# Kernel optimization log

Hardware: AMD Instinct MI355X
Metric: run time of the kernel (lower is better)

## Reference

```python
import jax, jax.numpy as jnp
import numpy as np

N = 100000  # nodes
E = 1600000  # edges
D_IN, D_HID, D_OUT = 128, 128, 64
NEG_SLOPE = 0.2


def gat_conv(x, src, dst, W_src, W_dst, att_src, att_dst, bias, num_nodes):
    # PyG GATConv, heads=1, add_self_loops=False.
    h_src = x @ W_src          # [N, C]
    h_dst = x @ W_dst          # [N, C]
    a_src = (h_src * att_src).sum(-1)   # [N]
    a_dst = (h_dst * att_dst).sum(-1)   # [N]
    logits = jax.nn.leaky_relu(a_src[src] + a_dst[dst], NEG_SLOPE)  # [E]
    # segment softmax over destination neighborhoods
    seg_max = jax.ops.segment_max(logits, dst, num_segments=num_nodes)  # [N]
    e = jnp.exp(logits - seg_max[dst])
    denom = jax.ops.segment_sum(e, dst, num_segments=num_nodes)         # [N]
    alpha = e / (denom[dst] + 1e-16)                                    # [E]
    out = jax.ops.segment_sum(alpha[:, None] * h_src[src], dst, num_segments=num_nodes)  # [N, C]
    return out + bias


def setup_inputs() -> dict:
    key = jax.random.key(0)
    ks = jax.random.split(key, 12)
    x = jax.random.normal(ks[0], (N, D_IN), dtype=jnp.float32)
    edge_index = jax.random.randint(ks[1], (2, E), 0, N, dtype=jnp.int64)
    s1 = 1.0 / np.sqrt(D_IN)
    s2 = 1.0 / np.sqrt(D_HID)
    return {
        "x": x,
        "edge_index": edge_index,
        "W1_src": jax.random.uniform(ks[2], (D_IN, D_HID), jnp.float32, -s1, s1),
        "W1_dst": jax.random.uniform(ks[3], (D_IN, D_HID), jnp.float32, -s1, s1),
        "att1_src": jax.random.uniform(ks[4], (D_HID,), jnp.float32, -s2, s2),
        "att1_dst": jax.random.uniform(ks[5], (D_HID,), jnp.float32, -s2, s2),
        "b1": jnp.zeros((D_HID,), jnp.float32),
        "W2_src": jax.random.uniform(ks[6], (D_HID, D_OUT), jnp.float32, -s2, s2),
        "W2_dst": jax.random.uniform(ks[7], (D_HID, D_OUT), jnp.float32, -s2, s2),
        "att2_src": jax.random.uniform(ks[8], (D_OUT,), jnp.float32, -1.0 / np.sqrt(D_OUT), 1.0 / np.sqrt(D_OUT)),
        "att2_dst": jax.random.uniform(ks[9], (D_OUT,), jnp.float32, -1.0 / np.sqrt(D_OUT), 1.0 / np.sqrt(D_OUT)),
        "b2": jnp.zeros((D_OUT,), jnp.float32),
    }


def reference(x, edge_index, W1_src, W1_dst, att1_src, att1_dst, b1,
              W2_src, W2_dst, att2_src, att2_dst, b2):
    src, dst = edge_index[0], edge_index[1]
    h = gat_conv(x, src, dst, W1_src, W1_dst, att1_src, att1_dst, b1, N)
    h = jax.nn.relu(h)
    out = gat_conv(h, src, dst, W2_src, W2_dst, att2_src, att2_dst, b2, N)
    return out
```

## Files before the change

kernel.cpp:

```cpp
#include <hip/hip_runtime.h>


typedef unsigned long long u64;
typedef float v4f __attribute__((ext_vector_type(4)));
typedef _Float16 v2h __attribute__((ext_vector_type(2)));
typedef __fp16 h8 __attribute__((ext_vector_type(8)));

#define SEL_LO 0x01000504u
#define SEL_HI 0x03020706u

__device__ __forceinline__ void ntstore4(float* p, v4f v) {
    __builtin_nontemporal_store(v, (v4f*)p);
}
__device__ __forceinline__ unsigned h2pack(float a, float b) {
    v2h h;
    h.x = (_Float16)a;
    h.y = (_Float16)b;
    return __builtin_bit_cast(unsigned, h);
}
__device__ __forceinline__ float fdot2u(unsigned u, v2h w, float acc) {
    return __builtin_amdgcn_fdot2(__builtin_bit_cast(v2h, u), w, acc, false);
}
__device__ __forceinline__ v2h pkrtz(float a, float b) {
    return __builtin_bit_cast(v2h, __builtin_amdgcn_cvt_pkrtz(a, b));
}

__global__ __launch_bounds__(64) void matvec_kernel(const float* __restrict__ W,
                                                    const float* __restrict__ a,
                                                    float* __restrict__ out, int cols) {
    int row = blockIdx.x;
    int lane = threadIdx.x;
    float s = 0.f;
    for (int j = lane; j < cols; j += 64) s += W[row * cols + j] * a[j];
#pragma unroll
    for (int o = 32; o; o >>= 1) s += __shfl_xor(s, o, 64);
    if (lane == 0) out[row] = s;
}

template <int C>
__global__ __launch_bounds__(256) void packw_kernel(const float* __restrict__ W,
                                                    uint4* __restrict__ Wp) {
    constexpr int NT = C / 16;
    const int total = 4 * NT * 64;
    for (int e = threadIdx.x; e < total; e += 256) {
        int lane = e & 63;
        int ti = (e >> 6) % NT;
        int t = (e >> 6) / NT;
        int k0 = 32 * t + (lane >> 4) * 8;
        int n = ti * 16 + (lane & 15);
        unsigned u[4];
#pragma unroll
        for (int p = 0; p < 4; ++p)
            u[p] = h2pack(W[(size_t)(k0 + 2 * p) * C + n], W[(size_t)(k0 + 2 * p + 1) * C + n]);
        Wp[e] = make_uint4(u[0], u[1], u[2], u[3]);
    }
}

__global__ __launch_bounds__(256) void bhist_kernel(const int* __restrict__ dst,
                                                    int* __restrict__ gh, int E) {
    __shared__ int h[256];
    h[threadIdx.x] = 0;
    __syncthreads();
    int base = blockIdx.x * 4096;
    int lim = min(base + 4096, E);
    for (int i = base + threadIdx.x; i < lim; i += 256)
        atomicAdd(&h[__builtin_nontemporal_load(dst + i) >> 9], 1);
    __syncthreads();
    int v = h[threadIdx.x];
    if (v) atomicAdd(&gh[threadIdx.x], v);
}

__global__ __launch_bounds__(256) void bscan_kernel(const int* __restrict__ gh,
                                                    int* __restrict__ bbase,
                                                    int* __restrict__ gcur,
                                                    int* __restrict__ offs, int N, int E) {
    __shared__ int s[256];
    int t = threadIdx.x;
    int v = gh[t];
    s[t] = v;
    __syncthreads();
    for (int o = 1; o < 256; o <<= 1) {
        int u = (t >= o) ? s[t - o] : 0;
        __syncthreads();
        s[t] += u;
        __syncthreads();
    }
    int excl = s[t] - v;
    bbase[t] = excl;
    gcur[t] = excl;
    if (t == 255) { bbase[256] = E; offs[N] = E; }
}

__global__ __launch_bounds__(256) void bscatter_kernel(const int* __restrict__ src,
                                                       const int* __restrict__ dst,
                                                       int* __restrict__ gcur,
                                                       u64* __restrict__ pairs, int E) {
    __shared__ int h[256];
    __shared__ int sbase[256];
    __shared__ int rbase[256];
    __shared__ u64 buf[4096];
    const int tid = threadIdx.x;
    h[tid] = 0;
    __syncthreads();
    const int base = blockIdx.x * 4096;
    const int lim = min(4096, E - base);
    u64 pv[16];
    int rk[16];
    int bk[16];
#pragma unroll 16
    for (int k = 0; k < 16; ++k) {
        int i = base + k * 256 + tid;
        if (i < E) {
            int d = __builtin_nontemporal_load(dst + i);
            int b = d >> 9;
            bk[k] = b;
            pv[k] = ((u64)(unsigned)d << 32) | (unsigned)__builtin_nontemporal_load(src + i);
            rk[k] = atomicAdd(&h[b], 1);
        } else {
            bk[k] = -1;
        }
    }
    __syncthreads();
    const int v = h[tid];
    sbase[tid] = v;
    __syncthreads();
    for (int o = 1; o < 256; o <<= 1) {
        int uu = (tid >= o) ? sbase[tid - o] : 0;
        __syncthreads();
        sbase[tid] += uu;
        __syncthreads();
    }
    const int excl = sbase[tid] - v;
    rbase[tid] = v ? atomicAdd(&gcur[tid], v) : 0;
    __syncthreads();
    sbase[tid] = excl;
    __syncthreads();
#pragma unroll 16
    for (int k = 0; k < 16; ++k)
        if (bk[k] >= 0) buf[sbase[bk[k]] + rk[k]] = pv[k];
    __syncthreads();
    for (int i = tid; i < lim; i += 256) {
        u64 p = buf[i];
        int b = (int)(p >> 41);
        __builtin_nontemporal_store(p, pairs + (size_t)rbase[b] + (i - sbase[b]));
    }
}

__global__ __launch_bounds__(512) void bsort_kernel(const u64* __restrict__ pairs,
                                                    const int* __restrict__ bbase,
                                                    int* __restrict__ offs,
                                                    int* __restrict__ srcs, int N) {
    __shared__ int h[512];
    __shared__ int cur[512];
    const int t = threadIdx.x;
    const int b = blockIdx.x;
    const int beg = bbase[b], end = bbase[b + 1];
    h[t] = 0;
    __syncthreads();
    for (int i = beg + t; i < end; i += 512)
        atomicAdd(&h[(int)(__builtin_nontemporal_load(pairs + i) >> 32) & 511], 1);
    __syncthreads();
    int v = h[t];
    cur[t] = v;
    __syncthreads();
    for (int o = 1; o < 512; o <<= 1) {
        int u = (t >= o) ? cur[t - o] : 0;
        __syncthreads();
        cur[t] += u;
        __syncthreads();
    }
    int pos0 = beg + cur[t] - v;
    __syncthreads();
    cur[t] = pos0;
    int g = (b << 9) + t;
    if (g < N) offs[g] = pos0;
    __syncthreads();
    for (int i = beg + t; i < end; i += 512) {
        u64 p = __builtin_nontemporal_load(pairs + i);
        int local = (int)(p >> 32) & 511;
        int pp = atomicAdd(&cur[local], 1);
        srcs[pp] = (int)(p & 0xffffffffu);
    }
}

template <int C, bool XF16>
__global__ __launch_bounds__(256) void gemm_att_kernel(
    const void* __restrict__ Xv, const uint4* __restrict__ Wp,
    const float* __restrict__ attS, const float* __restrict__ wda,
    unsigned* __restrict__ H, float* __restrict__ aS, float* __restrict__ aD, int M) {
    constexpr int NT = C / 16;
    __shared__ _Float16 hs[4][16 * 136];

    const int tid = threadIdx.x;
    const int w = tid >> 6;
    const int lane = tid & 63;
    const int l15 = lane & 15;
    const int q = lane >> 4;
    const int mb = blockIdx.x * 64 + w * 16;
    const int m = mb + l15;
    const bool mv = m < M;

    v4f acc[NT];
#pragma unroll
    for (int n = 0; n < NT; ++n) acc[n] = (v4f)(0.f);
    float pd = 0.f;
    uint4 afu[4];

    if constexpr (XF16) {
        const uint4* Xp = (const uint4*)Xv + (size_t)m * 16;
#pragma unroll
        for (int t = 0; t < 4; ++t) {
            uint4 u = make_uint4(0u, 0u, 0u, 0u);
            if (mv) u = Xp[4 * t + q];
            afu[t] = u;
            const float* wdp = wda + 32 * t + 8 * q;
            pd = fdot2u(u.x, pkrtz(wdp[0], wdp[1]), pd);
            pd = fdot2u(u.y, pkrtz(wdp[2], wdp[3]), pd);
            pd = fdot2u(u.z, pkrtz(wdp[4], wdp[5]), pd);
            pd = fdot2u(u.w, pkrtz(wdp[6], wdp[7]), pd);
        }
    } else {
        const float* Xp = (const float*)Xv + (size_t)m * 128;
#pragma unroll
        for (int t = 0; t < 4; ++t) {
            float4 x0 = make_float4(0.f, 0.f, 0.f, 0.f);
            float4 x1 = x0;
            if (mv) {
                x0 = *(const float4*)(Xp + 32 * t + 8 * q);
                x1 = *(const float4*)(Xp + 32 * t + 8 * q + 4);
            }
            const float* wdp = wda + 32 * t + 8 * q;
            pd += x0.x * wdp[0] + x0.y * wdp[1] + x0.z * wdp[2] + x0.w * wdp[3] +
                  x1.x * wdp[4] + x1.y * wdp[5] + x1.z * wdp[6] + x1.w * wdp[7];
            afu[t] = make_uint4(h2pack(x0.x, x0.y), h2pack(x0.z, x0.w),
                                h2pack(x1.x, x1.y), h2pack(x1.z, x1.w));
        }
    }

#pragma unroll
    for (int t = 0; t < 4; ++t) {
        h8 a = __builtin_bit_cast(h8, afu[t]);
        const uint4* wp = Wp + (size_t)t * NT * 64 + lane;
#pragma unroll
        for (int n = 0; n < NT; ++n) {
            h8 b = __builtin_bit_cast(h8, wp[n * 64]);
            acc[n] = __builtin_amdgcn_mfma_f32_16x16x32_f16(a, b, acc[n], 0, 0, 0);
        }
    }

    pd += __shfl_xor(pd, 16, 64);
    pd += __shfl_xor(pd, 32, 64);
    if (q == 0 && mv) aD[m] = pd;

    float as4[4] = {0.f, 0.f, 0.f, 0.f};
#pragma unroll
    for (int n = 0; n < NT; ++n) {
        float av = attS[n * 16 + l15];
#pragma unroll
        for (int r = 0; r < 4; ++r) as4[r] += acc[n][r] * av;
    }
#pragma unroll
    for (int r = 0; r < 4; ++r) {
#pragma unroll
        for (int o = 1; o < 16; o <<= 1) as4[r] += __shfl_xor(as4[r], o, 64);
    }
    if (l15 == 0) {
#pragma unroll
        for (int r = 0; r < 4; ++r) {
            int row = mb + q * 4 + r;
            if (row < M) aS[row] = as4[r];
        }
    }

    _Float16* hp = hs[w];
#pragma unroll
    for (int n = 0; n < NT; ++n)
#pragma unroll
        for (int r = 0; r < 4; ++r)
            hp[(q * 4 + r) * 136 + n * 16 + l15] = (_Float16)acc[n][r];

    constexpr int CH = C / 32;
    if (lane < 16 * CH) {
        int row = lane / CH;
        int ch = lane % CH;
        const uint4* rp = (const uint4*)(hp + row * 136 + ch * 32);
        uint4 v0 = rp[0], v1 = rp[1], v2 = rp[2], v3 = rp[3];
        int gr = mb + row;
        if (gr < M) {
            uint4* op = (uint4*)(H + (size_t)gr * (C / 2)) + ch * 4;
            op[0] = v0; op[1] = v1; op[2] = v2; op[3] = v3;
        }
    }
}

template <int C, bool RELU, bool F16OUT, bool NTOUT>
__global__ __launch_bounds__(256) void aggregate_kernel(
    const int* __restrict__ offs, const int* __restrict__ srcs,
    const unsigned* __restrict__ hsrc, const float* __restrict__ aS,
    const float* __restrict__ aD, const float* __restrict__ bias,
    void* __restrict__ outv, int n) {
    const int lane = threadIdx.x & 63;
    const int sl = lane & 31;
    const int hb = lane & 32;
    const int g = (lane >> 4) & 1;
    const int l = lane & 15;
    int node = (int)((blockIdx.x * blockDim.x + threadIdx.x) >> 5);
    if (node >= n) return;

    const int beg = offs[node], end = offs[node + 1];
    const int deg = end - beg;
    const float ad = aD[node];

    constexpr int LW = C / 32;
    constexpr int NA = C / 16;
    float acc[NA];
#pragma unroll
    for (int i = 0; i < NA; ++i) acc[i] = 0.f;

    int sj = 0;
    float u = 0.f;

    auto ldrow = [&](int s, unsigned* r) {
        if constexpr (C == 128) {
            uint4 v = ((const uint4*)(hsrc + ((size_t)s << 6)))[l];
            r[0] = v.x; r[1] = v.y; r[2] = v.z; r[3] = v.w;
        } else {
            uint2 v = ((const uint2*)(hsrc + ((size_t)s << 5)))[l];
            r[0] = v.x; r[1] = v.y;
        }
    };
    auto issue = [&](int j, unsigned (*buf)[LW]) {
        int e0 = hb + j * 8 + g;
        int s0 = __shfl(sj, e0, 64);
        int s1 = __shfl(sj, e0 + 2, 64);
        int s2 = __shfl(sj, e0 + 4, 64);
        int s3 = __shfl(sj, e0 + 6, 64);
        ldrow(s0, buf[0]);
        ldrow(s1, buf[1]);
        ldrow(s2, buf[2]);
        ldrow(s3, buf[3]);
    };
    auto compute = [&](int j, unsigned (*buf)[LW], float inv) {
        int e0 = hb + j * 8 + g;
        float w0 = __shfl(u, e0, 64) * inv, w1 = __shfl(u, e0 + 2, 64) * inv;
        float w2 = __shfl(u, e0 + 4, 64) * inv, w3 = __shfl(u, e0 + 6, 64) * inv;
        v2h w01 = pkrtz(w0, w1);
        v2h w23 = pkrtz(w2, w3);
#pragma unroll
        for (int ii = 0; ii < LW; ++ii) {
            acc[2 * ii] = fdot2u(__builtin_amdgcn_perm(buf[0][ii], buf[1][ii], SEL_LO), w01,
                          fdot2u(__builtin_amdgcn_perm(buf[2][ii], buf[3][ii], SEL_LO), w23, acc[2 * ii]));
            acc[2 * ii + 1] = fdot2u(__builtin_amdgcn_perm(buf[0][ii], buf[1][ii], SEL_HI), w01,
                              fdot2u(__builtin_amdgcn_perm(buf[2][ii], buf[3][ii], SEL_HI), w23, acc[2 * ii + 1]));
        }
    };

    unsigned A0[4][LW], A1[4][LW], A2[4][LW], A3[4][LW];

    if (deg <= 32) {
        int i = beg + sl;
        if (i < end) sj = __builtin_nontemporal_load(srcs + i);
        float asv = (i < end) ? aS[sj] : 0.f;
        int jm = (deg + 7) >> 3;
        if (jm > 0) issue(0, A0);
        if (jm > 1) issue(1, A1);
        if (jm > 2) issue(2, A2);
        if (jm > 3) issue(3, A3);
        if (i < end) {
            float lg = asv + ad;
            lg = (lg > 0.f) ? lg : 0.2f * lg;
            u = __expf(lg);
        }
        float s = u;
#pragma unroll
        for (int o = 16; o; o >>= 1) s += __shfl_xor(s, o, 64);
        float inv = 1.f / (s + 1e-16f);
        if (jm > 0) compute(0, A0, inv);
        if (jm > 1) compute(1, A1, inv);
        if (jm > 2) compute(2, A2, inv);
        if (jm > 3) compute(3, A3, inv);
    } else {
        float m = -INFINITY;
        for (int i = beg + sl; i < end; i += 32) {
            float lg = aS[srcs[i]] + ad;
            lg = (lg > 0.f) ? lg : 0.2f * lg;
            m = fmaxf(m, lg);
        }
#pragma unroll
        for (int o = 16; o; o >>= 1) m = fmaxf(m, __shfl_xor(m, o, 64));
        float ssum = 0.f;
        for (int i = beg + sl; i < end; i += 32) {
            float lg = aS[srcs[i]] + ad;
            lg = (lg > 0.f) ? lg : 0.2f * lg;
            ssum += __expf(lg - m);
        }
#pragma unroll
        for (int o = 16; o; o >>= 1) ssum += __shfl_xor(ssum, o, 64);
        float inv = 1.f / (ssum + 1e-16f);
        for (int base = beg; base < end; base += 32) {
            int i = base + sl;
            sj = 0;
            u = 0.f;
            if (i < end) {
                sj = srcs[i];
                float lg = aS[sj] + ad;
                lg = (lg > 0.f) ? lg : 0.2f * lg;
                u = __expf(lg - m);
            }
            int cnt = min(32, end - base);
            int cj = (cnt + 7) >> 3;
            if (cj > 0) issue(0, A0);
            if (cj > 1) issue(1, A1);
            if (cj > 2) issue(2, A2);
            if (cj > 3) issue(3, A3);
            if (cj > 0) compute(0, A0, inv);
            if (cj > 1) compute(1, A1, inv);
            if (cj > 2) compute(2, A2, inv);
            if (cj > 3) compute(3, A3, inv);
        }
    }

#pragma unroll
    for (int i = 0; i < NA; ++i) acc[i] += __shfl_xor(acc[i], 16, 64);

    if (sl < 16) {
        float o[NA];
        const float* bp = bias + l * NA;
#pragma unroll
        for (int i = 0; i < NA; ++i) {
            o[i] = acc[i] + bp[i];
            if (RELU) o[i] = fmaxf(o[i], 0.f);
        }
        if constexpr (F16OUT) {
            unsigned uo[NA / 2];
#pragma unroll
            for (int k = 0; k < NA / 2; ++k) uo[k] = h2pack(o[2 * k], o[2 * k + 1]);
            unsigned* op = (unsigned*)outv + (size_t)node * (C / 2) + l * (NA / 2);
            if constexpr (NA == 8) *(uint4*)op = make_uint4(uo[0], uo[1], uo[2], uo[3]);
            else *(uint2*)op = make_uint2(uo[0], uo[1]);
        } else {
            float* op = (float*)outv + (size_t)node * C + l * NA;
#pragma unroll
            for (int q = 0; q < NA / 4; ++q) {
                v4f ov;
                ov.x = o[q * 4 + 0]; ov.y = o[q * 4 + 1];
                ov.z = o[q * 4 + 2]; ov.w = o[q * 4 + 3];
                if (NTOUT) ntstore4(op + q * 4, ov);
                else *(v4f*)(op + q * 4) = ov;
            }
        }
    }
}

extern "C" void kernel_launch(void* const* d_in, const int* in_sizes, int n_in,
                              void* d_out, int out_size, void* d_ws, size_t ws_size,
                              hipStream_t stream) {
    const float* x     = (const float*)d_in[0];
    const int*   edge  = (const int*)d_in[1];
    const float* W1s   = (const float*)d_in[2];
    const float* W1d   = (const float*)d_in[3];
    const float* att1s = (const float*)d_in[4];
    const float* att1d = (const float*)d_in[5];
    const float* b1    = (const float*)d_in[6];
    const float* W2s   = (const float*)d_in[7];
    const float* W2d   = (const float*)d_in[8];
    const float* att2s = (const float*)d_in[9];
    const float* att2d = (const float*)d_in[10];
    const float* b2    = (const float*)d_in[11];

    const int N = in_sizes[0] / 128;
    const int E = in_sizes[1] / 2;
    const int* srcI = edge;
    const int* dstI = edge + E;

    size_t off = 0;
    auto alloc = [&](size_t bytes) {
        void* p = (char*)d_ws + off;
        off += (bytes + 255) & ~(size_t)255;
        return p;
    };
    int*      offs  = (int*)alloc((size_t)(N + 1) * 4);
    int*      srcs  = (int*)alloc((size_t)E * 4);
    int*      gh    = (int*)alloc(256 * 4);
    int*      bbase = (int*)alloc(257 * 4);
    int*      gcur  = (int*)alloc(256 * 4);
    float*    watt1 = (float*)alloc(128 * 4);
    float*    watt2 = (float*)alloc(128 * 4);
    uint4*    wp1   = (uint4*)alloc(4 * 8 * 64 * 16);
    uint4*    wp2   = (uint4*)alloc(4 * 4 * 64 * 16);
    float*    a_s   = (float*)alloc((size_t)N * 4);
    float*    a_d   = (float*)alloc((size_t)N * 4);
    unsigned* g1h   = (unsigned*)alloc((size_t)N * 128 * 2);
    unsigned* h1h   = (unsigned*)alloc((size_t)N * 128 * 2);
    unsigned* g2h   = (unsigned*)alloc((size_t)N * 64 * 2);
    u64*      pairs = (u64*)h1h;

    hipMemsetAsync(gh, 0, 256 * 4, stream);
    matvec_kernel<<<128, 64, 0, stream>>>(W1d, att1d, watt1, 128);
    matvec_kernel<<<128, 64, 0, stream>>>(W2d, att2d, watt2, 64);
    packw_kernel<128><<<1, 256, 0, stream>>>(W1s, wp1);
    packw_kernel<64><<<1, 256, 0, stream>>>(W2s, wp2);

    const int nbE = (E + 4095) / 4096;
    const int nbuckets = (N + 511) >> 9;
    bhist_kernel<<<nbE, 256, 0, stream>>>(dstI, gh, E);
    bscan_kernel<<<1, 256, 0, stream>>>(gh, bbase, gcur, offs, N, E);
    bscatter_kernel<<<nbE, 256, 0, stream>>>(srcI, dstI, gcur, pairs, E);
    bsort_kernel<<<nbuckets, 512, 0, stream>>>(pairs, bbase, offs, srcs, N);

    int gblk = (N + 63) / 64;
    gemm_att_kernel<128, false><<<gblk, 256, 0, stream>>>(x, wp1, att1s, watt1, g1h, a_s, a_d, N);
    aggregate_kernel<128, true, true, false><<<(N + 7) / 8, 256, 0, stream>>>(
        offs, srcs, g1h, a_s, a_d, b1, h1h, N);
    gemm_att_kernel<64, true><<<gblk, 256, 0, stream>>>(h1h, wp2, att2s, watt2, g2h, a_s, a_d, N);
    aggregate_kernel<64, false, false, true><<<(N + 7) / 8, 256, 0, stream>>>(
        offs, srcs, g2h, a_s, a_d, b2, d_out, N);
}
```

Before: 312.0 us.

## Merge setup kernels, co-launch scatter with GEMM, recompute source attention in aggregate

Folds the histogram, weight packing and matvec launches into one setup kernel that writes per-block histograms instead of using global atomics and a memset; the scan now sums those partial histograms. The edge scatter and the first-layer GEMM are fused into one launch with a shared-memory union, so they can overlap. In the low-degree aggregate path, the source attention logit is recomputed as an fp16 dot product over the gathered feature row instead of a separate gather of aS. This cuts launch count and one random gather, at the cost of extra dot-product work and fp16 precision in the attention logits.

```diff
diff --git a/kernel.cpp b/kernel.cpp
--- a/kernel.cpp
+++ b/kernel.cpp
@@ -25,11 +25,9 @@
     return __builtin_bit_cast(v2h, __builtin_amdgcn_cvt_pkrtz(a, b));
 }
 
-__global__ __launch_bounds__(64) void matvec_kernel(const float* __restrict__ W,
-                                                    const float* __restrict__ a,
-                                                    float* __restrict__ out, int cols) {
-    int row = blockIdx.x;
-    int lane = threadIdx.x;
+__device__ void matvec_body(const float* __restrict__ W, const float* __restrict__ a,
+                            float* __restrict__ out, int cols, int row) {
+    int lane = threadIdx.x & 63;
     float s = 0.f;
     for (int j = lane; j < cols; j += 64) s += W[row * cols + j] * a[j];
 #pragma unroll
@@ -38,8 +36,7 @@
 }
 
 template <int C>
-__global__ __launch_bounds__(256) void packw_kernel(const float* __restrict__ W,
-                                                    uint4* __restrict__ Wp) {
+__device__ void packw_body(const float* __restrict__ W, uint4* __restrict__ Wp) {
     constexpr int NT = C / 16;
     const int total = 4 * NT * 64;
     for (int e = threadIdx.x; e < total; e += 256) {
@@ -56,27 +53,43 @@
     }
 }
 
-__global__ __launch_bounds__(256) void bhist_kernel(const int* __restrict__ dst,
-                                                    int* __restrict__ gh, int E) {
-    __shared__ int h[256];
-    h[threadIdx.x] = 0;
-    __syncthreads();
-    int base = blockIdx.x * 4096;
-    int lim = min(base + 4096, E);
-    for (int i = base + threadIdx.x; i < lim; i += 256)
-        atomicAdd(&h[__builtin_nontemporal_load(dst + i) >> 9], 1);
-    __syncthreads();
-    int v = h[threadIdx.x];
-    if (v) atomicAdd(&gh[threadIdx.x], v);
-}
-
-__global__ __launch_bounds__(256) void bscan_kernel(const int* __restrict__ gh,
+__global__ __launch_bounds__(256) void setup_kernel(
+    const int* __restrict__ dst, int* __restrict__ hist, int E, int nbE,
+    const float* __restrict__ W1s, uint4* __restrict__ wp1,
+    const float* __restrict__ W2s, uint4* __restrict__ wp2,
+    const float* __restrict__ W1d, const float* __restrict__ att1d, float* __restrict__ watt1,
+    const float* __restrict__ W2d, const float* __restrict__ att2d, float* __restrict__ watt2) {
+    int b = blockIdx.x;
+    if (b < nbE) {
+        __shared__ int h[256];
+        h[threadIdx.x] = 0;
+        __syncthreads();
+        int base = b * 4096;
+        int lim = min(base + 4096, E);
+        for (int i = base + threadIdx.x; i < lim; i += 256)
+            atomicAdd(&h[__builtin_nontemporal_load(dst + i) >> 9], 1);
+        __syncthreads();
+        __builtin_nontemporal_store(h[threadIdx.x], hist + b * 256 + threadIdx.x);
+    } else if (b == nbE) {
+        packw_body<128>(W1s, wp1);
+    } else if (b == nbE + 1) {
+        packw_body<64>(W2s, wp2);
+    } else if (b < nbE + 34) {
+        matvec_body(W1d, att1d, watt1, 128, (b - nbE - 2) * 4 + (threadIdx.x >> 6));
+    } else {
+        matvec_body(W2d, att2d, watt2, 64, (b - nbE - 34) * 4 + (threadIdx.x >> 6));
+    }
+}
+
+__global__ __launch_bounds__(256) void bscan_kernel(const int* __restrict__ hist, int nbE,
                                                     int* __restrict__ bbase,
                                                     int* __restrict__ gcur,
                                                     int* __restrict__ offs, int N, int E) {
     __shared__ int s[256];
     int t = threadIdx.x;
-    int v = gh[t];
+    int v = 0;
+#pragma unroll 4
+    for (int b = 0; b < nbE; ++b) v += hist[b * 256 + t];
     s[t] = v;
     __syncthreads();
     for (int o = 1; o < 256; o <<= 1) {
@@ -91,18 +104,17 @@
     if (t == 255) { bbase[256] = E; offs[N] = E; }
 }
 
-__global__ __launch_bounds__(256) void bscatter_kernel(const int* __restrict__ src,
-                                                       const int* __restrict__ dst,
-                                                       int* __restrict__ gcur,
-                                                       u64* __restrict__ pairs, int E) {
-    __shared__ int h[256];
-    __shared__ int sbase[256];
-    __shared__ int rbase[256];
-    __shared__ u64 buf[4096];
+__device__ void scatter_body(const int* __restrict__ src, const int* __restrict__ dst,
+                             int* __restrict__ gcur, u64* __restrict__ pairs, int E,
+                             int blk, char* smem) {
+    int* h = (int*)smem;
+    int* sbase = h + 256;
+    int* rbase = h + 512;
+    u64* buf = (u64*)(smem + 3072);
     const int tid = threadIdx.x;
     h[tid] = 0;
     __syncthreads();
-    const int base = blockIdx.x * 4096;
+    const int base = blk * 4096;
     const int lim = min(4096, E - base);
     u64 pv[16];
     int rk[16];
@@ -184,19 +196,17 @@
 }
 
 template <int C, bool XF16>
-__global__ __launch_bounds__(256) void gemm_att_kernel(
-    const void* __restrict__ Xv, const uint4* __restrict__ Wp,
-    const float* __restrict__ attS, const float* __restrict__ wda,
-    unsigned* __restrict__ H, float* __restrict__ aS, float* __restrict__ aD, int M) {
+__device__ void gemm_body(int blk, const void* __restrict__ Xv, const uint4* __restrict__ Wp,
+                          const float* __restrict__ attS, const float* __restrict__ wda,
+                          unsigned* __restrict__ H, float* __restrict__ aS,
+                          float* __restrict__ aD, int M, _Float16* hsAll) {
     constexpr int NT = C / 16;
-    __shared__ _Float16 hs[4][16 * 136];
-
     const int tid = threadIdx.x;
     const int w = tid >> 6;
     const int lane = tid & 63;
     const int l15 = lane & 15;
     const int q = lane >> 4;
-    const int mb = blockIdx.x * 64 + w * 16;
+    const int mb = blk * 64 + w * 16;
     const int m = mb + l15;
     const bool mv = m < M;
 
@@ -272,7 +282,7 @@
         }
     }
 
-    _Float16* hp = hs[w];
+    _Float16* hp = hsAll + w * (16 * 136);
 #pragma unroll
     for (int n = 0; n < NT; ++n)
 #pragma unroll
@@ -293,12 +303,33 @@
     }
 }
 
+template <int C, bool XF16>
+__global__ __launch_bounds__(256) void gemm_att_kernel(
+    const void* __restrict__ Xv, const uint4* __restrict__ Wp,
+    const float* __restrict__ attS, const float* __restrict__ wda,
+    unsigned* __restrict__ H, float* __restrict__ aS, float* __restrict__ aD, int M) {
+    __shared__ _Float16 hs[4 * 16 * 136];
+    gemm_body<C, XF16>(blockIdx.x, Xv, Wp, attS, wda, H, aS, aD, M, hs);
+}
+
+__global__ __launch_bounds__(256) void scatter_gemm_kernel(
+    const int* __restrict__ src, const int* __restrict__ dst, int* __restrict__ gcur,
+    u64* __restrict__ pairs, int E, int nbS,
+    const void* __restrict__ Xv, const uint4* __restrict__ Wp,
+    const float* __restrict__ attS, const float* __restrict__ wda,
+    unsigned* __restrict__ H, float* __restrict__ aS, float* __restrict__ aD, int M) {
+    __shared__ __align__(16) char smem[35840];
+    int b = blockIdx.x;
+    if (b < nbS) scatter_body(src, dst, gcur, pairs, E, b, smem);
+    else gemm_body<128, false>(b - nbS, Xv, Wp, attS, wda, H, aS, aD, M, (_Float16*)smem);
+}
+
 template <int C, bool RELU, bool F16OUT, bool NTOUT>
 __global__ __launch_bounds__(256) void aggregate_kernel(
     const int* __restrict__ offs, const int* __restrict__ srcs,
-    const unsigned* __restrict__ hsrc, const float* __restrict__ aS,
-    const float* __restrict__ aD, const float* __restrict__ bias,
-    void* __restrict__ outv, int n) {
+    const unsigned* __restrict__ hsrc, const float* __restrict__ attS,
+    const float* __restrict__ aS, const float* __restrict__ aD,
+    const float* __restrict__ bias, void* __restrict__ outv, int n) {
     const int lane = threadIdx.x & 63;
     const int sl = lane & 31;
     const int hb = lane & 32;
@@ -316,6 +347,14 @@
     float acc[NA];
 #pragma unroll
     for (int i = 0; i < NA; ++i) acc[i] = 0.f;
+
+    v2h ash[LW];
+    {
+        const float* ap = attS + l * (2 * LW);
+#pragma unroll
+        for (int k = 0; k < LW; ++k)
+            ash[k] = __builtin_bit_cast(v2h, h2pack(ap[2 * k], ap[2 * k + 1]));
+    }
 
     int sj = 0;
     float u = 0.f;
@@ -340,12 +379,32 @@
         ldrow(s2, buf[2]);
         ldrow(s3, buf[3]);
     };
-    auto compute = [&](int j, unsigned (*buf)[LW], float inv) {
-        int e0 = hb + j * 8 + g;
-        float w0 = __shfl(u, e0, 64) * inv, w1 = __shfl(u, e0 + 2, 64) * inv;
-        float w2 = __shfl(u, e0 + 4, 64) * inv, w3 = __shfl(u, e0 + 6, 64) * inv;
-        v2h w01 = pkrtz(w0, w1);
-        v2h w23 = pkrtz(w2, w3);
+
+    auto edot = [&](int j, unsigned (*buf)[LW]) -> float {
+        float d0 = 0.f, d1 = 0.f, d2 = 0.f, d3 = 0.f;
+#pragma unroll
+        for (int k = 0; k < LW; ++k) {
+            d0 = fdot2u(buf[0][k], ash[k], d0);
+            d1 = fdot2u(buf[1][k], ash[k], d1);
+            d2 = fdot2u(buf[2][k], ash[k], d2);
+            d3 = fdot2u(buf[3][k], ash[k], d3);
+        }
+        bool h8 = (l & 8) != 0;
+        float a = (h8 ? d1 : d0) + __shfl_xor(h8 ? d0 : d1, 8, 64);
+        float b = (h8 ? d3 : d2) + __shfl_xor(h8 ? d2 : d3, 8, 64);
+        bool h4 = (l & 4) != 0;
+        float c = (h4 ? b : a) + __shfl_xor(h4 ? a : b, 4, 64);
+        c += __shfl_xor(c, 2, 64);
+        c += __shfl_xor(c, 1, 64);
+        int bsel = ((l >> 3) & 1) | (((l >> 2) & 1) << 1);
+        int slot = j * 8 + g + 2 * bsel;
+        float lg = c + ad;
+        lg = (lg > 0.f) ? lg : 0.2f * lg;
+        float uu = __expf(lg);
+        return (slot < deg) ? uu : 0.f;
+    };
+
+    auto dotacc = [&](unsigned (*buf)[LW], v2h w01, v2h w23) {
 #pragma unroll
         for (int ii = 0; ii < LW; ++ii) {
             acc[2 * ii] = fdot2u(__builtin_amdgcn_perm(buf[0][ii], buf[1][ii], SEL_LO), w01,
@@ -355,30 +414,46 @@
         }
     };
 
+    auto computeF = [&](unsigned (*buf)[LW], float uj, float inv) {
+        int bse = lane & 48;
+        float w0 = __shfl(uj, bse + 0, 64) * inv;
+        float w1 = __shfl(uj, bse + 8, 64) * inv;
+        float w2 = __shfl(uj, bse + 4, 64) * inv;
+        float w3 = __shfl(uj, bse + 12, 64) * inv;
+        dotacc(buf, pkrtz(w0, w1), pkrtz(w2, w3));
+    };
+
+    auto computeS = [&](int j, unsigned (*buf)[LW], float inv) {
+        int e0 = hb + j * 8 + g;
+        float w0 = __shfl(u, e0, 64) * inv, w1 = __shfl(u, e0 + 2, 64) * inv;
+        float w2 = __shfl(u, e0 + 4, 64) * inv, w3 = __shfl(u, e0 + 6, 64) * inv;
+        dotacc(buf, pkrtz(w0, w1), pkrtz(w2, w3));
+    };
+
     unsigned A0[4][LW], A1[4][LW], A2[4][LW], A3[4][LW];
 
     if (deg <= 32) {
         int i = beg + sl;
         if (i < end) sj = __builtin_nontemporal_load(srcs + i);
-        float asv = (i < end) ? aS[sj] : 0.f;
         int jm = (deg + 7) >> 3;
         if (jm > 0) issue(0, A0);
         if (jm > 1) issue(1, A1);
         if (jm > 2) issue(2, A2);
         if (jm > 3) issue(3, A3);
-        if (i < end) {
-            float lg = asv + ad;
-            lg = (lg > 0.f) ? lg : 0.2f * lg;
-            u = __expf(lg);
-        }
-        float s = u;
-#pragma unroll
-        for (int o = 16; o; o >>= 1) s += __shfl_xor(s, o, 64);
-        float inv = 1.f / (s + 1e-16f);
-        if (jm > 0) compute(0, A0, inv);
-        if (jm > 1) compute(1, A1, inv);
-        if (jm > 2) compute(2, A2, inv);
-        if (jm > 3) compute(3, A3, inv);
+        float u0 = 0.f, u1 = 0.f, u2 = 0.f, u3 = 0.f;
+        if (jm > 0) u0 = edot(0, A0);
+        if (jm > 1) u1 = edot(1, A1);
+        if (jm > 2) u2 = edot(2, A2);
+        if (jm > 3) u3 = edot(3, A3);
+        float t = (u0 + u1) + (u2 + u3);
+        t += __shfl_xor(t, 8, 64);
+        t += __shfl_xor(t, 4, 64);
+        t += __shfl_xor(t, 16, 64);
+        float inv = 1.f / (t + 1e-16f);
+        if (jm > 0) computeF(A0, u0, inv);
+        if (jm > 1) computeF(A1, u1, inv);
+        if (jm > 2) computeF(A2, u2, inv);
+        if (jm > 3) computeF(A3, u3, inv);
     } else {
         float m = -INFINITY;
         for (int i = beg + sl; i < end; i += 32) {
@@ -413,10 +488,10 @@
             if (cj > 1) issue(1, A1);
             if (cj > 2) issue(2, A2);
             if (cj > 3) issue(3, A3);
-            if (cj > 0) compute(0, A0, inv);
-            if (cj > 1) compute(1, A1, inv);
-            if (cj > 2) compute(2, A2, inv);
-            if (cj > 3) compute(3, A3, inv);
+            if (cj > 0) computeS(0, A0, inv);
+            if (cj > 1) computeS(1, A1, inv);
+            if (cj > 2) computeS(2, A2, inv);
+            if (cj > 3) computeS(3, A3, inv);
         }
     }
 
@@ -473,6 +548,10 @@
     const int* srcI = edge;
     const int* dstI = edge + E;
 
+    const int nbE = (E + 4095) / 4096;
+    const int nbuckets = (N + 511) >> 9;
+    const int gblk = (N + 63) / 64;
+
     size_t off = 0;
     auto alloc = [&](size_t bytes) {
         void* p = (char*)d_ws + off;
@@ -481,7 +560,7 @@
     };
     int*      offs  = (int*)alloc((size_t)(N + 1) * 4);
     int*      srcs  = (int*)alloc((size_t)E * 4);
-    int*      gh    = (int*)alloc(256 * 4);
+    int*      hist  = (int*)alloc((size_t)nbE * 256 * 4);
     int*      bbase = (int*)alloc(257 * 4);
     int*      gcur  = (int*)alloc(256 * 4);
     float*    watt1 = (float*)alloc(128 * 4);
@@ -495,24 +574,15 @@
     unsigned* g2h   = (unsigned*)alloc((size_t)N * 64 * 2);
     u64*      pairs = (u64*)h1h;
 
-    hipMemsetAsync(gh, 0, 256 * 4, stream);
-    matvec_kernel<<<128, 64, 0, stream>>>(W1d, att1d, watt1, 128);
-    matvec_kernel<<<128, 64, 0, stream>>>(W2d, att2d, watt2, 64);
-    packw_kernel<128><<<1, 256, 0, stream>>>(W1s, wp1);
-    packw_kernel<64><<<1, 256, 0, stream>>>(W2s, wp2);
-
-    const int nbE = (E + 4095) / 4096;
-    const int nbuckets = (N + 511) >> 9;
-    bhist_kernel<<<nbE, 256, 0, stream>>>(dstI, gh, E);
-    bscan_kernel<<<1, 256, 0, stream>>>(gh, bbase, gcur, offs, N, E);
-    bscatter_kernel<<<nbE, 256, 0, stream>>>(srcI, dstI, gcur, pairs, E);
+    setup_kernel<<<nbE + 66, 256, 0, stream>>>(dstI, hist, E, nbE, W1s, wp1, W2s, wp2,
+                                               W1d, att1d, watt1, W2d, att2d, watt2);
+    bscan_kernel<<<1, 256, 0, stream>>>(hist, nbE, bbase, gcur, offs, N, E);
+    scatter_gemm_kernel<<<nbE + gblk, 256, 0, stream>>>(srcI, dstI, gcur, pairs, E, nbE,
+                                                        x, wp1, att1s, watt1, g1h, a_s, a_d, N);
     bsort_kernel<<<nbuckets, 512, 0, stream>>>(pairs, bbase, offs, srcs, N);
-
-    int gblk = (N + 63) / 64;
-    gemm_att_kernel<128, false><<<gblk, 256, 0, stream>>>(x, wp1, att1s, watt1, g1h, a_s, a_d, N);
     aggregate_kernel<128, true, true, false><<<(N + 7) / 8, 256, 0, stream>>>(
-        offs, srcs, g1h, a_s, a_d, b1, h1h, N);
+        offs, srcs, g1h, att1s, a_s, a_d, b1, h1h, N);
     gemm_att_kernel<64, true><<<gblk, 256, 0, stream>>>(h1h, wp2, att2s, watt2, g2h, a_s, a_d, N);
     aggregate_kernel<64, false, false, true><<<(N + 7) / 8, 256, 0, stream>>>(
-        offs, srcs, g2h, a_s, a_d, b2, d_out, N);
-}
+        offs, srcs, g2h, att2s, a_s, a_d, b2, d_out, N);
+}
```

Result: slower. 329.1 us (+5.5%).
